# Performance work log

Hardware: AMD Instinct MI355X
Metric: run time of the kernel (lower is better)

Reference implementation:

```python
import jax, jax.numpy as jnp
import numpy as np

B, N, E, D = 4, 50000, 800000, 64


def setup_inputs() -> dict:
    key = jax.random.key(0)
    k_h, k_e, k_w1, k_w2 = jax.random.split(key, 4)
    s = 1.0 / np.sqrt(D)  # glorot-ish scale for 64x64 linear weights
    return {
        "t": jnp.zeros((1,), jnp.float32),
        "h": jax.random.normal(k_h, (B, N, D), jnp.float32),
        "edge_index": jax.random.randint(k_e, (2, E), 0, N, jnp.int32),
        "W1": jax.random.normal(k_w1, (D, D), jnp.float32) * s,
        "b1": jnp.zeros((D,), jnp.float32),
        "W2": jax.random.normal(k_w2, (D, D), jnp.float32) * s,
        "b2": jnp.zeros((D,), jnp.float32),
    }


def _gcn(x, row, col, norm, W, b, n_nodes):
    # x: (B, N, D). PyG GCNConv: linear (no bias) -> normalized gather/scatter -> +bias
    xw = jnp.einsum("bnd,de->bne", x, W)
    msg = xw[:, row, :] * norm[None, :, None]          # (B, E+N, D)
    agg = jax.vmap(lambda m: jax.ops.segment_sum(m, col, num_segments=n_nodes))(msg)
    return agg + b


def reference(t, h, edge_index, W1, b1, W2, b2):
    n_nodes = h.shape[1]
    loop = jnp.arange(n_nodes, dtype=edge_index.dtype)
    # add self-loops (PyG GCNConv default)
    row = jnp.concatenate([edge_index[0], loop])  # source nodes
    col = jnp.concatenate([edge_index[1], loop])  # target nodes
    # symmetric normalization D^{-1/2} (A+I) D^{-1/2}; degree counted on targets
    deg = jax.ops.segment_sum(jnp.ones_like(row, dtype=h.dtype), col, num_segments=n_nodes)
    dis = jnp.where(deg > 0, jax.lax.rsqrt(deg), 0.0)
    norm = dis[row] * dis[col]
    h = jnp.tanh(_gcn(h, row, col, norm, W1, b1, n_nodes))
    h = jnp.tanh(_gcn(h, row, col, norm, W2, b2, n_nodes))
    return h
```

## Files before the change

kernel.cpp:

```cpp
#include <hip/hip_runtime.h>
#include <math.h>

#define B_ 4
#define N_ 50000
#define E_ 800000
#define D_ 64
#define M_ (B_*N_)

typedef _Float16 h4 __attribute__((ext_vector_type(4)));
typedef _Float16 h8 __attribute__((ext_vector_type(8)));
typedef float    f4 __attribute__((ext_vector_type(4)));

__global__ __launch_bounds__(256) void k_count(const int* __restrict__ col, int* __restrict__ cnt) {
  int e = blockIdx.x * 256 + threadIdx.x;
  if (e < E_) atomicAdd(&cnt[col[e]], 1);
}

__global__ __launch_bounds__(1024) void k_scan_a(const int* __restrict__ cnt, int* __restrict__ part,
                                                 float* __restrict__ dis) {
  __shared__ int sd[1024];
  int i = blockIdx.x * 1024 + threadIdx.x;
  int v = (i < N_) ? cnt[i] : 0;
  if (i < N_) dis[i] = 1.0f / sqrtf((float)(v + 1));
  sd[threadIdx.x] = v;
  __syncthreads();
  for (int s = 512; s > 0; s >>= 1) {
    if (threadIdx.x < s) sd[threadIdx.x] += sd[threadIdx.x + s];
    __syncthreads();
  }
  if (threadIdx.x == 0) part[blockIdx.x] = sd[0];
}

__global__ __launch_bounds__(1024) void k_scan_c(const int* __restrict__ cnt, const int* __restrict__ part,
                                                 int* __restrict__ off, int* __restrict__ cur) {
  __shared__ int sd[1024];
  __shared__ int base_s;
  int i = blockIdx.x * 1024 + threadIdx.x;
  int v = (i < N_) ? cnt[i] : 0;
  if (threadIdx.x == 0) {
    int b = 0;
    for (int j = 0; j < (int)blockIdx.x; j++) b += part[j];
    base_s = b;
  }
  sd[threadIdx.x] = v;
  __syncthreads();
  for (int s = 1; s < 1024; s <<= 1) {
    int t = (threadIdx.x >= s) ? sd[threadIdx.x - s] : 0;
    __syncthreads();
    sd[threadIdx.x] += t;
    __syncthreads();
  }
  int incl = sd[threadIdx.x];
  if (i < N_) { off[i] = base_s + incl - v; cur[i] = 0; }
  if (i == N_ - 1) off[N_] = base_s + incl;
}

__global__ __launch_bounds__(256) void k_fill(const int* __restrict__ row, const int* __restrict__ col,
                                              const int* __restrict__ off, int* __restrict__ cur,
                                              const float* __restrict__ dis,
                                              int2* __restrict__ em) {
  int e = blockIdx.x * 256 + threadIdx.x;
  if (e < E_) {
    int c = col[e], r = row[e];
    int p = off[c] + atomicAdd(&cur[c], 1);
    float w = dis[r] * dis[c];
    em[p] = make_int2(r, __float_as_int(w));
  }
}

__global__ __launch_bounds__(256) void k_wfrag(const float* __restrict__ W1, const float* __restrict__ W2,
                                               h8* __restrict__ Wf1, h8* __restrict__ Wf2) {
  int t0 = threadIdx.x;
  for (int w = 0; w < 2; w++) {
    const float* W = w ? W2 : W1;
    h8* Wf = w ? Wf2 : Wf1;
    for (int p = 0; p < 2; p++) {
      int fid = p * 256 + t0;
      int khalf = fid >> 8;
      int rem = fid & 255;
      int tt = rem >> 6;
      int lane = rem & 63;
      int kq = lane >> 4, m = lane & 15;
      h8 v;
#pragma unroll
      for (int j = 0; j < 8; j++) {
        int k = khalf * 32 + kq * 8 + j;
        v[j] = (_Float16)W[k * 64 + tt * 16 + m];
      }
      Wf[fid] = v;
    }
  }
}

__global__ __launch_bounds__(256) void k_linear(const float* __restrict__ X,
                                                const h8* __restrict__ Wf,
                                                _Float16* __restrict__ Y) {
  int wv = blockIdx.x * 4 + (threadIdx.x >> 6);
  int lane = threadIdx.x & 63;
  int m = lane & 15, kq = lane >> 4;
  size_t r0 = (size_t)wv * 16;
  const float* xr = X + (r0 + m) * 64 + kq * 8;
  f4 f0 = *(const f4*)(xr);
  f4 f1 = *(const f4*)(xr + 4);
  f4 f2 = *(const f4*)(xr + 32);
  f4 f3 = *(const f4*)(xr + 36);
  h8 a0, a1;
#pragma unroll
  for (int j = 0; j < 4; j++) {
    a0[j] = (_Float16)f0[j]; a0[j + 4] = (_Float16)f1[j];
    a1[j] = (_Float16)f2[j]; a1[j + 4] = (_Float16)f3[j];
  }
  f4 acc[4];
#pragma unroll
  for (int t = 0; t < 4; t++) {
    h8 b0 = Wf[t * 64 + lane];
    h8 b1 = Wf[256 + t * 64 + lane];
    f4 c = {0.f, 0.f, 0.f, 0.f};
    c = __builtin_amdgcn_mfma_f32_16x16x32_f16(a0, b0, c, 0, 0, 0);
    c = __builtin_amdgcn_mfma_f32_16x16x32_f16(a1, b1, c, 0, 0, 0);
    acc[t] = c;
  }
  int b  = (int)(r0 / N_);
  int n0 = (int)(r0 - (size_t)b * N_);
#pragma unroll
  for (int t = 0; t < 4; t++) {
#pragma unroll
    for (int r = 0; r < 4; r++) {
      int n = n0 + kq * 4 + r;
      Y[(size_t)n * 256 + b * 64 + t * 16 + m] = (_Float16)acc[t][r];
    }
  }
}

__global__ __launch_bounds__(256) void k_agg(const _Float16* __restrict__ xw,
                                             const int* __restrict__ off,
                                             const int2* __restrict__ em,
                                             const float* __restrict__ dis,
                                             const float* __restrict__ bias,
                                             float* __restrict__ out) {
  int node = blockIdx.x * 4 + (threadIdx.x >> 6);
  int lane = threadIdx.x & 63;
  if (node >= N_) return;
  const h4* xp = (const h4*)xw;
  float d  = dis[node];
  float sw = d * d;
  f4 acc = __builtin_convertvector(xp[(size_t)node * 64 + lane], f4) * sw;
  int s = off[node], e = off[node + 1];
  while (s < e) {
    int i = s + lane;
    int2 mm = (i < e) ? em[i] : make_int2(0, 0);
    int er = mm.x;
    float wn = __int_as_float(mm.y);
    int c = e - s; if (c > 64) c = 64;
    int c8 = (c + 7) & ~7;
    for (int j = 0; j < c8; j += 8) {
      int   s0 = __shfl(er, j),     s1 = __shfl(er, j + 1);
      int   s2 = __shfl(er, j + 2), s3 = __shfl(er, j + 3);
      int   s4 = __shfl(er, j + 4), s5 = __shfl(er, j + 5);
      int   s6 = __shfl(er, j + 6), s7 = __shfl(er, j + 7);
      float w0 = __shfl(wn, j),     w1 = __shfl(wn, j + 1);
      float w2 = __shfl(wn, j + 2), w3 = __shfl(wn, j + 3);
      float w4 = __shfl(wn, j + 4), w5 = __shfl(wn, j + 5);
      float w6 = __shfl(wn, j + 6), w7 = __shfl(wn, j + 7);
      h4 v0 = xp[(size_t)s0 * 64 + lane];
      h4 v1 = xp[(size_t)s1 * 64 + lane];
      h4 v2 = xp[(size_t)s2 * 64 + lane];
      h4 v3 = xp[(size_t)s3 * 64 + lane];
      h4 v4 = xp[(size_t)s4 * 64 + lane];
      h4 v5 = xp[(size_t)s5 * 64 + lane];
      h4 v6 = xp[(size_t)s6 * 64 + lane];
      h4 v7 = xp[(size_t)s7 * 64 + lane];
      acc += __builtin_convertvector(v0, f4) * w0;
      acc += __builtin_convertvector(v1, f4) * w1;
      acc += __builtin_convertvector(v2, f4) * w2;
      acc += __builtin_convertvector(v3, f4) * w3;
      acc += __builtin_convertvector(v4, f4) * w4;
      acc += __builtin_convertvector(v5, f4) * w5;
      acc += __builtin_convertvector(v6, f4) * w6;
      acc += __builtin_convertvector(v7, f4) * w7;
    }
    s += 64;
  }
  int b  = lane >> 4;
  int d0 = (lane & 15) * 4;
  f4 bb = *(const f4*)(bias + d0);
  f4 r;
  r.x = tanhf(acc.x + bb.x);
  r.y = tanhf(acc.y + bb.y);
  r.z = tanhf(acc.z + bb.z);
  r.w = tanhf(acc.w + bb.w);
  *(f4*)(out + (size_t)b * N_ * 64 + (size_t)node * 64 + d0) = r;
}

extern "C" void kernel_launch(void* const* d_in, const int* in_sizes, int n_in,
                              void* d_out, int out_size, void* d_ws, size_t ws_size,
                              hipStream_t stream) {
  const float* h  = (const float*)d_in[1];
  const int*   ei = (const int*)d_in[2];
  const float* W1 = (const float*)d_in[3];
  const float* b1 = (const float*)d_in[4];
  const float* W2 = (const float*)d_in[5];
  const float* b2 = (const float*)d_in[6];
  float* out = (float*)d_out;
  const int* row = ei;
  const int* col = ei + E_;

  char* p = (char*)d_ws;
  _Float16* xw = (_Float16*)p; p += (size_t)M_ * D_ * sizeof(_Float16);
  int2* em  = (int2*)p;   p += (size_t)E_ * sizeof(int2);
  int*  cnt = (int*)p;    p += (size_t)N_ * sizeof(int);
  int*  off = (int*)p;    p += (size_t)(N_ + 4) * sizeof(int);
  int*  cur = (int*)p;    p += (size_t)N_ * sizeof(int);
  float* dis = (float*)p; p += (size_t)N_ * sizeof(float);
  int*  prt = (int*)p;    p += 64 * sizeof(int);
  h8*   Wf1 = (h8*)p;     p += 512 * sizeof(h8);
  h8*   Wf2 = (h8*)p;     p += 512 * sizeof(h8);
  float* h1 = out;

  hipMemsetAsync(cnt, 0, N_ * sizeof(int), stream);

  k_count<<<(E_ + 255) / 256, 256, 0, stream>>>(col, cnt);
  int nscan = (N_ + 1023) / 1024;
  k_scan_a<<<nscan, 1024, 0, stream>>>(cnt, prt, dis);
  k_scan_c<<<nscan, 1024, 0, stream>>>(cnt, prt, off, cur);
  k_fill<<<(E_ + 255) / 256, 256, 0, stream>>>(row, col, off, cur, dis, em);
  k_wfrag<<<1, 256, 0, stream>>>(W1, W2, Wf1, Wf2);

  k_linear<<<M_ / 64, 256, 0, stream>>>(h, Wf1, xw);
  k_agg<<<N_ / 4, 256, 0, stream>>>(xw, off, em, dis, b1, h1);
  k_linear<<<M_ / 64, 256, 0, stream>>>(h1, Wf2, xw);
  k_agg<<<N_ / 4, 256, 0, stream>>>(xw, off, em, dis, b2, out);
}
```

Measured before the change: 336.8 us.

## Widen aggregation gathers to 16-byte half-wave loads, store intermediate in fp16

The aggregation kernel now has each half-wave gather one neighbor's full 512-byte row as 16-byte h8 loads. The two halves process alternating groups of 8 edges and are combined with a cross-lane xor shuffle, which doubles the number of edges in flight per wave. The first layer's output is written as fp16 so the second linear kernel reads half the bytes. Edge counting now reads col as int4 vectors. The costs are more registers per lane (8 accumulators, 8 h8 values), a wider launch_bounds occupancy hint, and an extra fp16 rounding of the intermediate activation.

```diff
diff --git a/kernel.cpp b/kernel.cpp
--- a/kernel.cpp
+++ b/kernel.cpp
@@ -11,9 +11,15 @@
 typedef _Float16 h8 __attribute__((ext_vector_type(8)));
 typedef float    f4 __attribute__((ext_vector_type(4)));
 
-__global__ __launch_bounds__(256) void k_count(const int* __restrict__ col, int* __restrict__ cnt) {
+__global__ __launch_bounds__(256) void k_count(const int4* __restrict__ col4, int* __restrict__ cnt) {
   int e = blockIdx.x * 256 + threadIdx.x;
-  if (e < E_) atomicAdd(&cnt[col[e]], 1);
+  if (e < E_ / 4) {
+    int4 c = col4[e];
+    atomicAdd(&cnt[c.x], 1);
+    atomicAdd(&cnt[c.y], 1);
+    atomicAdd(&cnt[c.z], 1);
+    atomicAdd(&cnt[c.w], 1);
+  }
 }
 
 __global__ __launch_bounds__(1024) void k_scan_a(const int* __restrict__ cnt, int* __restrict__ part,
@@ -92,23 +98,30 @@
   }
 }
 
-__global__ __launch_bounds__(256) void k_linear(const float* __restrict__ X,
+template<int IN_F16>
+__global__ __launch_bounds__(256) void k_linear(const void* __restrict__ Xv,
                                                 const h8* __restrict__ Wf,
                                                 _Float16* __restrict__ Y) {
   int wv = blockIdx.x * 4 + (threadIdx.x >> 6);
   int lane = threadIdx.x & 63;
   int m = lane & 15, kq = lane >> 4;
   size_t r0 = (size_t)wv * 16;
-  const float* xr = X + (r0 + m) * 64 + kq * 8;
-  f4 f0 = *(const f4*)(xr);
-  f4 f1 = *(const f4*)(xr + 4);
-  f4 f2 = *(const f4*)(xr + 32);
-  f4 f3 = *(const f4*)(xr + 36);
   h8 a0, a1;
-#pragma unroll
-  for (int j = 0; j < 4; j++) {
-    a0[j] = (_Float16)f0[j]; a0[j + 4] = (_Float16)f1[j];
-    a1[j] = (_Float16)f2[j]; a1[j + 4] = (_Float16)f3[j];
+  if constexpr (IN_F16) {
+    const _Float16* xr = (const _Float16*)Xv + (r0 + m) * 64 + kq * 8;
+    a0 = *(const h8*)(xr);
+    a1 = *(const h8*)(xr + 32);
+  } else {
+    const float* xr = (const float*)Xv + (r0 + m) * 64 + kq * 8;
+    f4 f0 = *(const f4*)(xr);
+    f4 f1 = *(const f4*)(xr + 4);
+    f4 f2 = *(const f4*)(xr + 32);
+    f4 f3 = *(const f4*)(xr + 36);
+#pragma unroll
+    for (int j = 0; j < 4; j++) {
+      a0[j] = (_Float16)f0[j]; a0[j + 4] = (_Float16)f1[j];
+      a1[j] = (_Float16)f2[j]; a1[j + 4] = (_Float16)f3[j];
+    }
   }
   f4 acc[4];
 #pragma unroll
@@ -132,19 +145,27 @@
   }
 }
 
-__global__ __launch_bounds__(256) void k_agg(const _Float16* __restrict__ xw,
-                                             const int* __restrict__ off,
-                                             const int2* __restrict__ em,
-                                             const float* __restrict__ dis,
-                                             const float* __restrict__ bias,
-                                             float* __restrict__ out) {
+template<int OUT_F16>
+__global__ __launch_bounds__(256, 8) void k_agg(const _Float16* __restrict__ xw,
+                                                const int* __restrict__ off,
+                                                const int2* __restrict__ em,
+                                                const float* __restrict__ dis,
+                                                const float* __restrict__ bias,
+                                                void* __restrict__ outv) {
   int node = blockIdx.x * 4 + (threadIdx.x >> 6);
   int lane = threadIdx.x & 63;
   if (node >= N_) return;
-  const h4* xp = (const h4*)xw;
+  int l5   = lane & 31;
+  int hsel = (lane >> 5) << 3;
+  const h8* xp = (const h8*)xw;
   float d  = dis[node];
   float sw = d * d;
-  f4 acc = __builtin_convertvector(xp[(size_t)node * 64 + lane], f4) * sw;
+  float acc[8] = {0, 0, 0, 0, 0, 0, 0, 0};
+  if (lane < 32) {
+    h8 sv = xp[(size_t)node * 32 + l5];
+#pragma unroll
+    for (int q = 0; q < 8; q++) acc[q] = (float)sv[q] * sw;
+  }
   int s = off[node], e = off[node + 1];
   while (s < e) {
     int i = s + lane;
@@ -152,44 +173,51 @@
     int er = mm.x;
     float wn = __int_as_float(mm.y);
     int c = e - s; if (c > 64) c = 64;
-    int c8 = (c + 7) & ~7;
-    for (int j = 0; j < c8; j += 8) {
-      int   s0 = __shfl(er, j),     s1 = __shfl(er, j + 1);
-      int   s2 = __shfl(er, j + 2), s3 = __shfl(er, j + 3);
-      int   s4 = __shfl(er, j + 4), s5 = __shfl(er, j + 5);
-      int   s6 = __shfl(er, j + 6), s7 = __shfl(er, j + 7);
-      float w0 = __shfl(wn, j),     w1 = __shfl(wn, j + 1);
-      float w2 = __shfl(wn, j + 2), w3 = __shfl(wn, j + 3);
-      float w4 = __shfl(wn, j + 4), w5 = __shfl(wn, j + 5);
-      float w6 = __shfl(wn, j + 6), w7 = __shfl(wn, j + 7);
-      h4 v0 = xp[(size_t)s0 * 64 + lane];
-      h4 v1 = xp[(size_t)s1 * 64 + lane];
-      h4 v2 = xp[(size_t)s2 * 64 + lane];
-      h4 v3 = xp[(size_t)s3 * 64 + lane];
-      h4 v4 = xp[(size_t)s4 * 64 + lane];
-      h4 v5 = xp[(size_t)s5 * 64 + lane];
-      h4 v6 = xp[(size_t)s6 * 64 + lane];
-      h4 v7 = xp[(size_t)s7 * 64 + lane];
-      acc += __builtin_convertvector(v0, f4) * w0;
-      acc += __builtin_convertvector(v1, f4) * w1;
-      acc += __builtin_convertvector(v2, f4) * w2;
-      acc += __builtin_convertvector(v3, f4) * w3;
-      acc += __builtin_convertvector(v4, f4) * w4;
-      acc += __builtin_convertvector(v5, f4) * w5;
-      acc += __builtin_convertvector(v6, f4) * w6;
-      acc += __builtin_convertvector(v7, f4) * w7;
+    for (int j = 0; j < c; j += 16) {
+      int sn[8]; float w[8];
+#pragma unroll
+      for (int k = 0; k < 8; k++) {
+        int sl = j + hsel + k;
+        sn[k] = __shfl(er, sl);
+        w[k]  = __shfl(wn, sl);
+      }
+      h8 v[8];
+#pragma unroll
+      for (int k = 0; k < 8; k++) v[k] = xp[(size_t)sn[k] * 32 + l5];
+#pragma unroll
+      for (int k = 0; k < 8; k++) {
+        float wk = w[k];
+#pragma unroll
+        for (int q = 0; q < 8; q++) acc[q] += (float)v[k][q] * wk;
+      }
     }
     s += 64;
   }
-  int b  = lane >> 4;
-  int d0 = (lane & 15) * 4;
-  f4 bb = *(const f4*)(bias + d0);
-  f4 r;
-  r.x = tanhf(acc.x + bb.x);
-  r.y = tanhf(acc.y + bb.y);
-  r.z = tanhf(acc.z + bb.z);
-  r.w = tanhf(acc.w + bb.w);
-  *(f4*)(out + (size_t)b * N_ * 64 + (size_t)node * 64 + d0) = r;
+#pragma unroll
+  for (int q = 0; q < 8; q++) acc[q] += __shfl_xor(acc[q], 32);
+  if (lane < 32) {
+    int b  = l5 >> 3;
+    int d0 = (l5 & 7) * 8;
+    f4 blo = *(const f4*)(bias + d0);
+    f4 bhi = *(const f4*)(bias + d0 + 4);
+    float r[8];
+#pragma unroll
+    for (int q = 0; q < 4; q++) r[q]     = tanhf(acc[q]     + blo[q]);
+#pragma unroll
+    for (int q = 0; q < 4; q++) r[q + 4] = tanhf(acc[q + 4] + bhi[q]);
+    if constexpr (OUT_F16) {
+      h8 o;
+#pragma unroll
+      for (int q = 0; q < 8; q++) o[q] = (_Float16)r[q];
+      *(h8*)((_Float16*)outv + ((size_t)b * N_ + node) * 64 + d0) = o;
+    } else {
+      float* op = (float*)outv + ((size_t)b * N_ + node) * 64 + d0;
+      f4 lo = {r[0], r[1], r[2], r[3]};
+      f4 hi = {r[4], r[5], r[6], r[7]};
+      *(f4*)op       = lo;
+      *(f4*)(op + 4) = hi;
+    }
+  }
 }
 
 extern "C" void kernel_launch(void* const* d_in, const int* in_sizes, int n_in,
@@ -215,19 +243,19 @@
   int*  prt = (int*)p;    p += 64 * sizeof(int);
   h8*   Wf1 = (h8*)p;     p += 512 * sizeof(h8);
   h8*   Wf2 = (h8*)p;     p += 512 * sizeof(h8);
-  float* h1 = out;
+  _Float16* h1 = (_Float16*)d_out;
 
   hipMemsetAsync(cnt, 0, N_ * sizeof(int), stream);
 
-  k_count<<<(E_ + 255) / 256, 256, 0, stream>>>(col, cnt);
+  k_count<<<(E_ / 4 + 255) / 256, 256, 0, stream>>>((const int4*)col, cnt);
   int nscan = (N_ + 1023) / 1024;
   k_scan_a<<<nscan, 1024, 0, stream>>>(cnt, prt, dis);
   k_scan_c<<<nscan, 1024, 0, stream>>>(cnt, prt, off, cur);
   k_fill<<<(E_ + 255) / 256, 256, 0, stream>>>(row, col, off, cur, dis, em);
   k_wfrag<<<1, 256, 0, stream>>>(W1, W2, Wf1, Wf2);
 
-  k_linear<<<M_ / 64, 256, 0, stream>>>(h, Wf1, xw);
-  k_agg<<<N_ / 4, 256, 0, stream>>>(xw, off, em, dis, b1, h1);
-  k_linear<<<M_ / 64, 256, 0, stream>>>(h1, Wf2, xw);
-  k_agg<<<N_ / 4, 256, 0, stream>>>(xw, off, em, dis, b2, out);
-}
+  k_linear<0><<<M_ / 64, 256, 0, stream>>>(h, Wf1, xw);
+  k_agg<1><<<N_ / 4, 256, 0, stream>>>(xw, off, em, dis, b1, h1);
+  k_linear<1><<<M_ / 64, 256, 0, stream>>>(h1, Wf2, xw);
+  k_agg<0><<<N_ / 4, 256, 0, stream>>>(xw, off, em, dis, b2, out);
+}
```

After: 393.0 us. 16.7% more time.
